# Optimization experiments

Measured on AMD Instinct MI355X. Metric: run time of the kernel, lower is better.

Reference implementation:

```python
import jax, jax.numpy as jnp
import numpy as np

B, N, D = 1, 10000, 256
NH, PT, PP, PS = 8, 4, 4, 4
DFF, NC, HF, WF = 1024, 6, 24, 60
BH, BW = 100, 100
T_RAD, S_RAD = 0.15, 0.12


def setup_inputs() -> dict:
    key = jax.random.key(0)
    ks = jax.random.split(key, 20)
    p = lambda i, shape: jax.random.normal(ks[i], shape, jnp.float32) * 0.02
    return {
        "query": jax.random.normal(ks[0], (B, N, D), jnp.float32),
        "prev_bev": jax.random.normal(ks[1], (B, N, D), jnp.float32),
        "image_feats": jax.random.normal(ks[2], (B, NC, D, HF, WF), jnp.float32),
        "reference_points_2d": jax.random.uniform(ks[3], (B, N, 2), jnp.float32),
        "reference_points_cam": jax.random.uniform(ks[4], (B, NC, N, PP, 2), jnp.float32),
        "ego_shift": jax.random.normal(ks[5], (B, 2), jnp.float32) * 0.02,
        "t_off_w": p(6, (2 * D, 2 * NH * PT * 2)), "t_off_b": jnp.zeros((2 * NH * PT * 2,)),
        "t_wt_w": p(7, (2 * D, 2 * NH * PT)), "t_wt_b": jnp.zeros((2 * NH * PT,)),
        "t_out_w": p(8, (D, D)), "t_out_b": jnp.zeros((D,)),
        "s_off_w": p(9, (D, NH * PP * PS * 2)), "s_off_b": jnp.zeros((NH * PP * PS * 2,)),
        "s_wt_w": p(10, (D, NH * PP * PS)), "s_wt_b": jnp.zeros((NH * PP * PS,)),
        "s_out_w": p(11, (D, D)), "s_out_b": jnp.zeros((D,)),
        "ffn_w1": p(12, (D, DFF)), "ffn_b1": jnp.zeros((DFF,)),
        "ffn_w2": p(13, (DFF, D)), "ffn_b2": jnp.zeros((D,)),
        "ln1_g": jnp.ones((D,)), "ln1_b": jnp.zeros((D,)),
        "ln2_g": jnp.ones((D,)), "ln2_b": jnp.zeros((D,)),
        "ln3_g": jnp.ones((D,)), "ln3_b": jnp.zeros((D,)),
        "bev_mask": jax.random.bernoulli(ks[14], 0.7, (B, NC, N, PP)),
        "bev_h": BH, "bev_w": BW,
    }


def _ln(x, g, b):
    mu = x.mean(-1, keepdims=True)
    var = ((x - mu) ** 2).mean(-1, keepdims=True)
    return (x - mu) / jnp.sqrt(var + 1e-5) * g + b


def _masked_softmax(logits, mask):
    m = mask.astype(logits.dtype)
    w = jax.nn.softmax(jnp.where(m == 0, -1e9, logits), axis=-1) * m
    return w / jnp.maximum(w.sum(-1, keepdims=True), 1e-6)


def _bilinear(feat, grid):
    # feat: [G, C, H, W]; grid: [G, Q, P, 2] in [-1, 1] (x, y); align_corners=False, zero pad
    G, C, H, W = feat.shape
    ix = ((grid[..., 0] + 1.0) * W - 1.0) * 0.5
    iy = ((grid[..., 1] + 1.0) * H - 1.0) * 0.5
    x0 = jnp.floor(ix); y0 = jnp.floor(iy)
    wx1 = ix - x0; wy1 = iy - y0
    feat_flat = feat.reshape(G, C, H * W)
    def corner(xc, yc, w):
        valid = (xc >= 0) & (xc < W) & (yc >= 0) & (yc < H)
        xi = jnp.clip(xc, 0, W - 1).astype(jnp.int32)
        yi = jnp.clip(yc, 0, H - 1).astype(jnp.int32)
        idx = (yi * W + xi).reshape(G, -1)
        vals = jax.vmap(lambda f, i: f[:, i])(feat_flat, idx)  # [G, C, Q*P]
        return vals * (w * valid.astype(feat.dtype)).reshape(G, 1, -1)
    out = (corner(x0, y0, (1 - wx1) * (1 - wy1)) + corner(x0 + 1, y0, wx1 * (1 - wy1))
           + corner(x0, y0 + 1, (1 - wx1) * wy1) + corner(x0 + 1, y0 + 1, wx1 * wy1))
    return out.reshape(G, C, grid.shape[1], grid.shape[2])


def _sample(fmap, pts, nh):
    # fmap: [B, C, H, W]; pts: [B, N, nh, P, 2] in [0, 1] -> [B, N, nh, P, hd]
    b, c, h, w = fmap.shape
    _, n, _, p, _ = pts.shape
    hd = c // nh
    feat = fmap.reshape(b * nh, hd, h, w)
    grid = jnp.transpose(pts, (0, 2, 1, 3, 4)).reshape(b * nh, n, p, 2) * 2.0 - 1.0
    s = _bilinear(feat, grid).reshape(b, nh, hd, n, p)
    return jnp.transpose(s, (0, 3, 1, 4, 2))


def _forward(query, prev_bev, image_feats, ref2d, refcam, ego_shift,
             t_off_w, t_off_b, t_wt_w, t_wt_b, t_out_w, t_out_b,
             s_off_w, s_off_b, s_wt_w, s_wt_b, s_out_w, s_out_b,
             ffn_w1, ffn_b1, ffn_w2, ffn_b2,
             ln1_g, ln1_b, ln2_g, ln2_b, ln3_g, ln3_b,
             bev_mask, bev_h, bev_w):
    b, n, d = query.shape
    nc = image_feats.shape[1]
    # ---- temporal self attention (pre-norm) ----
    q1 = _ln(query, ln1_g, ln1_b)
    pb = _ln(prev_bev, ln1_g, ln1_b)
    cur_map = jnp.transpose(q1, (0, 2, 1)).reshape(b, d, bev_h, bev_w)
    prev_map = jnp.transpose(pb, (0, 2, 1)).reshape(b, d, bev_h, bev_w)
    ai = jnp.concatenate([pb, q1], -1)
    toff = jnp.tanh(ai @ t_off_w + t_off_b).reshape(b, n, 2, NH, PT, 2) * T_RAD
    twl = (ai @ t_wt_w + t_wt_b).reshape(b, n, 2, NH, PT)
    base = jnp.stack([ref2d + ego_shift[:, None, :], ref2d], axis=2)
    t_outs = []
    for si, smap in enumerate((prev_map, cur_map)):
        loc = base[:, :, si, None, None, :] + toff[:, :, si]  # [b,n,NH,PT,2]
        w = jax.nn.softmax(twl[:, :, si], -1)
        s = _sample(smap, loc, NH)
        t_outs.append((s * w[..., None]).sum(3))  # [b,n,NH,hd]
    t_fused = ((t_outs[0] + t_outs[1]) * 0.5).reshape(b, n, d)
    x = query + (t_fused @ t_out_w + t_out_b)
    # ---- spatial cross attention (pre-norm) ----
    q2 = _ln(x, ln2_g, ln2_b)
    soff = jnp.tanh(q2 @ s_off_w + s_off_b).reshape(b, n, NH, PP, PS, 2) * S_RAD
    swl = (q2 @ s_wt_w + s_wt_b).reshape(b, n, NH, PP * PS)
    acc = jnp.zeros((b, n, d), query.dtype)
    cnt = jnp.zeros((b, n), query.dtype)
    for c in range(nc):
        ref = refcam[:, c]          # [b,n,PP,2]
        vis = bev_mask[:, c]        # [b,n,PP] bool
        loc = (ref[:, :, None, :, None, :] + soff).reshape(b, n, NH, PP * PS, 2)
        vm = jnp.broadcast_to(vis[:, :, None, :, None], (b, n, NH, PP, PS)).reshape(b, n, NH, PP * PS)
        w = _masked_softmax(swl, vm)
        s = _sample(image_feats[:, c], loc, NH)
        co = (s * w[..., None]).sum(3).reshape(b, n, d)
        hv = vis.any(-1)
        acc = acc + co * hv[..., None].astype(co.dtype)
        cnt = cnt + hv.astype(cnt.dtype)
    s_fused = acc / jnp.maximum(cnt, 1.0)[..., None]
    x = x + (s_fused @ s_out_w + s_out_b)
    # ---- FFN (pre-norm) ----
    h = jax.nn.relu(_ln(x, ln3_g, ln3_b) @ ffn_w1 + ffn_b1)
    return x + (h @ ffn_w2 + ffn_b2)


def reference(query, prev_bev, image_feats, reference_points_2d, reference_points_cam, ego_shift,
              t_off_w, t_off_b, t_wt_w, t_wt_b, t_out_w, t_out_b,
              s_off_w, s_off_b, s_wt_w, s_wt_b, s_out_w, s_out_b,
              ffn_w1, ffn_b1, ffn_w2, ffn_b2,
              ln1_g, ln1_b, ln2_g, ln2_b, ln3_g, ln3_b,
              bev_mask, bev_h, bev_w):
    return _forward(query, prev_bev, image_feats, reference_points_2d, reference_points_cam, ego_shift,
                    t_off_w, t_off_b, t_wt_w, t_wt_b, t_out_w, t_out_b,
                    s_off_w, s_off_b, s_wt_w, s_wt_b, s_out_w, s_out_b,
                    ffn_w1, ffn_b1, ffn_w2, ffn_b2,
                    ln1_g, ln1_b, ln2_g, ln2_b, ln3_g, ln3_b,
                    bev_mask, bev_h, bev_w)
```

## Files before the change

kernel.cpp:

```cpp
#include <hip/hip_runtime.h>
#include <hip/hip_bf16.h>
#include <hip/hip_fp16.h>

#define N_Q 10000
#define D_MODEL 256
#define NH 8
#define PT 4
#define PP 4
#define PS 4
#define DFF 1024
#define NC 6
#define HF 24
#define WF 60
#define BH 100
#define BW 100
#define T_RAD 0.15f
#define S_RAD 0.12f

typedef __hip_bfloat16 bf16;
typedef __attribute__((ext_vector_type(8))) short short8;
typedef __attribute__((ext_vector_type(4))) float f32x4;

__device__ __forceinline__ float b2f(bf16 v) { return __bfloat162float(v); }
__device__ __forceinline__ bf16 f2b(float v) { return __float2bfloat16(v); }

__device__ __forceinline__ f32x4 mfma16(short8 a, short8 b, f32x4 c) {
    return __builtin_amdgcn_mfma_f32_16x16x32_bf16(a, b, c, 0, 0, 0);
}

__device__ __forceinline__ float load_any(const void* p, long i, int f) {
    if (f == 0) return ((const float*)p)[i];
    if (f == 1) return b2f(((const bf16*)p)[i]);
    return __half2float(((const __half*)p)[i]);
}
__device__ __forceinline__ void store_any(void* p, long i, int f, float v) {
    if (f == 0)      ((float*)p)[i] = v;
    else if (f == 1) ((bf16*)p)[i] = f2b(v);
    else             ((__half*)p)[i] = __float2half(v);
}

__device__ __forceinline__ unsigned pack2(float a, float b) {
    bf16 x = f2b(a), y = f2b(b);
    unsigned short ux = *(unsigned short*)&x, uy = *(unsigned short*)&y;
    return (unsigned)ux | ((unsigned)uy << 16);
}

__global__ __launch_bounds__(256) void detect_kernel(const void* __restrict__ ln1g,
                                                     const void* __restrict__ mask,
                                                     int* __restrict__ flags) {
    __shared__ int sh[6];
    int tid = threadIdx.x;
    if (tid < 6) sh[tid] = (tid == 0 || tid == 2 || tid == 4) ? 1 : 0;
    __syncthreads();
    const unsigned long long* m64 = (const unsigned long long*)mask;
    const unsigned int*       m32 = (const unsigned int*)mask;
    const unsigned short*     m16 = (const unsigned short*)mask;
    int lok8 = 1, lones8 = 0, lok4 = 1, lones4 = 0, lok2 = 1, lones2 = 0;
    for (int i = tid; i < 480; i += 256) {
        if (i < 120) {
            unsigned long long v = m64[i];
            if (v == 1ULL) lones8++; else if (v != 0ULL) lok8 = 0;
        }
        if (i < 240) {
            unsigned int v = m32[i];
            if (v == 1u || v == 0x3F800000u) lones4++; else if (v != 0u) lok4 = 0;
        }
        unsigned short v = m16[i];
        if (v == 1 || v == 0x3F80) lones2++; else if (v != 0) lok2 = 0;
    }
    atomicAnd(&sh[0], lok8); atomicAdd(&sh[1], lones8);
    atomicAnd(&sh[2], lok4); atomicAdd(&sh[3], lones4);
    atomicAnd(&sh[4], lok2); atomicAdd(&sh[5], lones2);
    __syncthreads();
    if (tid == 0) {
        unsigned short u0 = ((const unsigned short*)ln1g)[0];
        flags[0] = (u0 == 0x3F80) ? 1 : (u0 == 0x3C00 ? 2 : 0);
        int ms;
        if (sh[0] && sh[1] > 30)       ms = 8;
        else if (sh[2] && sh[3] > 60)  ms = 4;
        else if (sh[4] && sh[5] > 120) ms = 2;
        else                           ms = 1;
        flags[1] = ms;
    }
}

#define NP 23
struct PrepDesc {
    const void* src[NP];
    int dst_off[NP];
    int count[NP];
    int R[NP];
    int C[NP];
    int type[NP];
    int blk_start[NP + 1];
};
__global__ __launch_bounds__(256) void prep_kernel(PrepDesc pd, bf16* __restrict__ wgt,
                                                   bf16* __restrict__ imgT,
                                                   const int* __restrict__ flags) {
    int blk = blockIdx.x;
    int a = 0;
    while (a < NP - 1 && blk >= pd.blk_start[a + 1]) a++;
    int i = (blk - pd.blk_start[a]) * 256 + threadIdx.x;
    if (i >= pd.count[a]) return;
    int f = flags[0];
    int ty = pd.type[a];
    if (ty == 0) {
        wgt[pd.dst_off[a] + i] = f2b(load_any(pd.src[a], i, f));
    } else if (ty == 1) {
        int R = pd.R[a], C = pd.C[a];
        int c = i / R, r = i % R;
        wgt[pd.dst_off[a] + i] = f2b(load_any(pd.src[a], (long)r * C + c, f));
    } else {
        int ch = i & 255;
        int t = i >> 8;
        int xx = t % WF; t /= WF;
        int yy = t % HF;
        int c  = t / HF;
        long src = (((long)(c * 256) + ch) * HF + yy) * WF + xx;
        imgT[i] = f2b(load_any(pd.src[a], src, f));
    }
}

__global__ __launch_bounds__(256) void ln12_kernel(const void* __restrict__ pb,
                                                   const void* __restrict__ q,
                                                   const int* __restrict__ flags,
                                                   const bf16* __restrict__ g,
                                                   const bf16* __restrict__ b,
                                                   bf16* __restrict__ out) {
    int wv = threadIdx.x >> 6, lane = threadIdx.x & 63;
    long row = (long)blockIdx.x * 4 + wv;
    const void* src; long r; int ooff;
    if (row < N_Q) { src = pb; r = row; ooff = 0; }
    else           { src = q;  r = row - N_Q; ooff = 256; }
    int f = flags[0];
    float v0, v1, v2, v3;
    if (f == 0) {
        float4 t = ((const float4*)src)[r * 64 + lane];
        v0 = t.x; v1 = t.y; v2 = t.z; v3 = t.w;
    } else {
        uint2 t = ((const uint2*)src)[r * 64 + lane];
        if (f == 1) {
            v0 = __uint_as_float(t.x << 16); v1 = __uint_as_float(t.x & 0xFFFF0000u);
            v2 = __uint_as_float(t.y << 16); v3 = __uint_as_float(t.y & 0xFFFF0000u);
        } else {
            __half2 h0 = *(__half2*)&t.x, h1 = *(__half2*)&t.y;
            v0 = __half2float(h0.x); v1 = __half2float(h0.y);
            v2 = __half2float(h1.x); v3 = __half2float(h1.y);
        }
    }
    float s1 = v0 + v1 + v2 + v3;
    float s2 = v0 * v0 + v1 * v1 + v2 * v2 + v3 * v3;
    #pragma unroll
    for (int m = 32; m > 0; m >>= 1) {
        s1 += __shfl_xor(s1, m);
        s2 += __shfl_xor(s2, m);
    }
    float mu = s1 * (1.f / 256.f);
    float var = s2 * (1.f / 256.f) - mu * mu;
    float inv = rsqrtf(var + 1e-5f);
    int k = lane * 4;
    float o0 = (v0 - mu) * inv * b2f(g[k+0]) + b2f(b[k+0]);
    float o1 = (v1 - mu) * inv * b2f(g[k+1]) + b2f(b[k+1]);
    float o2 = (v2 - mu) * inv * b2f(g[k+2]) + b2f(b[k+2]);
    float o3 = (v3 - mu) * inv * b2f(g[k+3]) + b2f(b[k+3]);
    uint2 st = {pack2(o0, o1), pack2(o2, o3)};
    *reinterpret_cast<uint2*>(out + r * 512 + ooff + k) = st;
}

__global__ __launch_bounds__(256) void ln_kernel(const float* __restrict__ in,
                                                 const bf16* __restrict__ g,
                                                 const bf16* __restrict__ b,
                                                 bf16* __restrict__ out) {
    int wv = threadIdx.x >> 6, lane = threadIdx.x & 63;
    long r = (long)blockIdx.x * 4 + wv;
    float4 t = ((const float4*)in)[r * 64 + lane];
    float s1 = t.x + t.y + t.z + t.w;
    float s2 = t.x * t.x + t.y * t.y + t.z * t.z + t.w * t.w;
    #pragma unroll
    for (int m = 32; m > 0; m >>= 1) {
        s1 += __shfl_xor(s1, m);
        s2 += __shfl_xor(s2, m);
    }
    float mu = s1 * (1.f / 256.f);
    float var = s2 * (1.f / 256.f) - mu * mu;
    float inv = rsqrtf(var + 1e-5f);
    int k = lane * 4;
    float o0 = (t.x - mu) * inv * b2f(g[k+0]) + b2f(b[k+0]);
    float o1 = (t.y - mu) * inv * b2f(g[k+1]) + b2f(b[k+1]);
    float o2 = (t.z - mu) * inv * b2f(g[k+2]) + b2f(b[k+2]);
    float o3 = (t.w - mu) * inv * b2f(g[k+3]) + b2f(b[k+3]);
    uint2 st = {pack2(o0, o1), pack2(o2, o3)};
    *reinterpret_cast<uint2*>(out + r * 256 + k) = st;
}

template <int K, int J, int MODE>
__global__ __launch_bounds__(256) void gemm_mfma(const bf16* __restrict__ A,
                                                 const bf16* __restrict__ WT,
                                                 const bf16* __restrict__ bias,
                                                 float* __restrict__ outf,
                                                 const void* __restrict__ resraw,
                                                 const float* __restrict__ resf,
                                                 const int* __restrict__ flags) {
    constexpr int LDK = K + 8;
    __shared__ bf16 As[32 * LDK];
    int tid = threadIdx.x;
    int row0 = blockIdx.x * 32;
    int col0 = blockIdx.y * 64;
    for (int t = tid; t < 32 * (K / 8); t += 256) {
        int r = t / (K / 8), kq = t % (K / 8);
        uint4 u = {0u, 0u, 0u, 0u};
        if (row0 + r < N_Q)
            u = *reinterpret_cast<const uint4*>(A + (size_t)(row0 + r) * K + kq * 8);
        *reinterpret_cast<uint4*>(&As[r * LDK + kq * 8]) = u;
    }
    __syncthreads();
    int wave = tid >> 6, lane = tid & 63;
    int l = lane & 15, quad = lane >> 4;
    int rh = wave >> 1, ch = wave & 1;
    constexpr int NK = K / 32;
    short8 afr[NK];
    const bf16* arow = &As[(rh * 16 + l) * LDK + quad * 8];
    #pragma unroll
    for (int ks = 0; ks < NK; ks++)
        afr[ks] = *reinterpret_cast<const short8*>(arow + ks * 32);
    int fdt = flags[0];
    #pragma unroll
    for (int ct = 0; ct < 2; ct++) {
        int col = col0 + ch * 32 + ct * 16 + l;
        const bf16* wrow = WT + (size_t)col * K + quad * 8;
        f32x4 acc = {0.f, 0.f, 0.f, 0.f};
        #pragma unroll
        for (int ks = 0; ks < NK; ks++) {
            short8 bfr = *reinterpret_cast<const short8*>(wrow + ks * 32);
            acc = mfma16(afr[ks], bfr, acc);
        }
        float bb = b2f(bias[col]);
        #pragma unroll
        for (int r = 0; r < 4; r++) {
            int row = row0 + rh * 16 + quad * 4 + r;
            if (row >= N_Q) continue;
            long o = (long)row * J + col;
            float v = acc[r] + bb;
            if (MODE == 2) outf[o] = v + load_any(resraw, o, fdt);
            else           outf[o] = v + resf[o];
        }
    }
}

template <int K, int J1, int J2>
__global__ __launch_bounds__(256) void gemm_dual(const bf16* __restrict__ A,
                                                 const bf16* __restrict__ WT1,
                                                 const bf16* __restrict__ b1, float scale,
                                                 bf16* __restrict__ out1,
                                                 const bf16* __restrict__ WT2,
                                                 const bf16* __restrict__ b2,
                                                 bf16* __restrict__ out2) {
    constexpr int LDK = K + 8;
    __shared__ bf16 As[32 * LDK];
    int tid = threadIdx.x;
    int row0 = blockIdx.x * 32;
    int col0 = blockIdx.y * 64;
    for (int t = tid; t < 32 * (K / 8); t += 256) {
        int r = t / (K / 8), kq = t % (K / 8);
        uint4 u = {0u, 0u, 0u, 0u};
        if (row0 + r < N_Q)
            u = *reinterpret_cast<const uint4*>(A + (size_t)(row0 + r) * K + kq * 8);
        *reinterpret_cast<uint4*>(&As[r * LDK + kq * 8]) = u;
    }
    __syncthreads();
    int wave = tid >> 6, lane = tid & 63;
    int l = lane & 15, quad = lane >> 4;
    int rh = wave >> 1, ch = wave & 1;
    constexpr int NK = K / 32;
    short8 afr[NK];
    const bf16* arow = &As[(rh * 16 + l) * LDK + quad * 8];
    #pragma unroll
    for (int ks = 0; ks < NK; ks++)
        afr[ks] = *reinterpret_cast<const short8*>(arow + ks * 32);
    #pragma unroll
    for (int ct = 0; ct < 2; ct++) {
        int jg = col0 + ch * 32 + ct * 16 + l;
        int in1 = jg < J1;
        int cl = in1 ? jg : jg - J1;
        const bf16* wrow = (in1 ? WT1 : WT2) + (size_t)cl * K + quad * 8;
        f32x4 acc = {0.f, 0.f, 0.f, 0.f};
        #pragma unroll
        for (int ks = 0; ks < NK; ks++) {
            short8 bfr = *reinterpret_cast<const short8*>(wrow + ks * 32);
            acc = mfma16(afr[ks], bfr, acc);
        }
        float bb = b2f(in1 ? b1[cl] : b2[cl]);
        #pragma unroll
        for (int r = 0; r < 4; r++) {
            int row = row0 + rh * 16 + quad * 4 + r;
            if (row >= N_Q) continue;
            float v = acc[r] + bb;
            if (in1) out1[(long)row * J1 + cl] = f2b(tanhf(v) * scale);
            else     out2[(long)row * J2 + cl] = f2b(v);
        }
    }
}

__global__ __launch_bounds__(256) void ffn_mfma(const float* __restrict__ x,
                                                const bf16* __restrict__ g3,
                                                const bf16* __restrict__ b3,
                                                const bf16* __restrict__ w1T,
                                                const bf16* __restrict__ b1,
                                                const bf16* __restrict__ w2T,
                                                const bf16* __restrict__ b2v,
                                                void* __restrict__ out,
                                                const int* __restrict__ flags) {
    constexpr int LDH = DFF + 8;
    constexpr int LDX = D_MODEL + 8;
    __shared__ bf16 hbuf[16 * LDH];
    bf16* xl = hbuf;
    int tid = threadIdx.x;
    int row0 = blockIdx.x * 16;
    {
        int r = tid >> 4, lr = tid & 15;
        const float* xr = x + (long)(row0 + r) * 256 + lr * 16;
        float vals[16];
        float s1 = 0.f, s2 = 0.f;
        #pragma unroll
        for (int i = 0; i < 16; i++) {
            float v = xr[i];
            vals[i] = v; s1 += v; s2 += v * v;
        }
        #pragma unroll
        for (int off = 8; off > 0; off >>= 1) {
            s1 += __shfl_down(s1, off, 16);
            s2 += __shfl_down(s2, off, 16);
        }
        s1 = __shfl(s1, 0, 16);
        s2 = __shfl(s2, 0, 16);
        float mu = s1 * (1.f / 256.f);
        float var = s2 * (1.f / 256.f) - mu * mu;
        float inv = rsqrtf(var + 1e-5f);
        #pragma unroll
        for (int i = 0; i < 16; i++) {
            int k = lr * 16 + i;
            xl[r * LDX + k] = f2b((vals[i] - mu) * inv * b2f(g3[k]) + b2f(b3[k]));
        }
    }
    __syncthreads();
    int wave = tid >> 6, lane = tid & 63;
    int l = lane & 15, quad = lane >> 4;
    short8 afr[8];
    {
        const bf16* arow = xl + l * LDX + quad * 8;
        #pragma unroll
        for (int ks = 0; ks < 8; ks++)
            afr[ks] = *reinterpret_cast<const short8*>(arow + ks * 32);
    }
    __syncthreads();
    for (int ct = 0; ct < 16; ct++) {
        int col = wave * 256 + ct * 16 + l;
        const bf16* wrow = w1T + (size_t)col * 256 + quad * 8;
        f32x4 acc = {0.f, 0.f, 0.f, 0.f};
        #pragma unroll
        for (int ks = 0; ks < 8; ks++) {
            short8 bfr = *reinterpret_cast<const short8*>(wrow + ks * 32);
            acc = mfma16(afr[ks], bfr, acc);
        }
        float bb = b2f(b1[col]);
        #pragma unroll
        for (int r = 0; r < 4; r++)
            hbuf[(quad * 4 + r) * LDH + col] = f2b(fmaxf(acc[r] + bb, 0.f));
    }
    __syncthreads();
    int fdt = flags[0];
    for (int ct = 0; ct < 4; ct++) {
        int col = wave * 64 + ct * 16 + l;
        const bf16* wrow = w2T + (size_t)col * 1024 + quad * 8;
        const bf16* hrow = hbuf + l * LDH + quad * 8;
        f32x4 acc = {0.f, 0.f, 0.f, 0.f};
        #pragma unroll 8
        for (int ks = 0; ks < 32; ks++) {
            short8 a2 = *reinterpret_cast<const short8*>(hrow + ks * 32);
            short8 bfr = *reinterpret_cast<const short8*>(wrow + ks * 32);
            acc = mfma16(a2, bfr, acc);
        }
        float bb = b2f(b2v[col]);
        #pragma unroll
        for (int r = 0; r < 4; r++) {
            long o = (long)(row0 + quad * 4 + r) * 256 + col;
            store_any(out, o, fdt, x[o] + acc[r] + bb);
        }
    }
}

__global__ __launch_bounds__(256) void temporal_kernel(const bf16* __restrict__ ai,
                                                       const bf16* __restrict__ toffB,
                                                       const bf16* __restrict__ twlB,
                                                       const void* __restrict__ ref2d,
                                                       const void* __restrict__ ego,
                                                       const int* __restrict__ flags,
                                                       bf16* __restrict__ tfB) {
    int tid = threadIdx.x;
    int ql = tid >> 5, t = tid & 31;
    int g = t >> 2, q4 = t & 3;
    long n0 = (long)blockIdx.x * 8;
    __shared__ float s_toff[8][8][17];
    __shared__ float s_twl[8][64];
    __shared__ float s_base[8][4];
    for (int i = tid; i < 8 * 128; i += 256) {
        int q = i >> 7, j = i & 127;
        int si = j >> 6, r = j & 63, gg = r >> 3, w = r & 7;
        s_toff[q][gg][si * 8 + w] = b2f(toffB[n0 * 128 + i]);
    }
    for (int i = tid; i < 8 * 64; i += 256) s_twl[i >> 6][i & 63] = b2f(twlB[n0 * 64 + i]);
    if (tid < 8) {
        int f = flags[0];
        float rx = load_any(ref2d, (n0 + tid) * 2, f), ry = load_any(ref2d, (n0 + tid) * 2 + 1, f);
        s_base[tid][0] = rx + load_any(ego, 0, f); s_base[tid][1] = ry + load_any(ego, 1, f);
        s_base[tid][2] = rx;                       s_base[tid][3] = ry;
    }
    __syncthreads();
    float acc[8];
    #pragma unroll
    for (int i = 0; i < 8; i++) acc[i] = 0.f;
    int choff = g * 32 + q4 * 8;
    #pragma unroll
    for (int si = 0; si < 2; si++) {
        float l0 = s_twl[ql][si * 32 + g * 4 + 0], l1 = s_twl[ql][si * 32 + g * 4 + 1];
        float l2 = s_twl[ql][si * 32 + g * 4 + 2], l3 = s_twl[ql][si * 32 + g * 4 + 3];
        float mx = fmaxf(fmaxf(l0, l1), fmaxf(l2, l3));
        float e0 = __expf(l0 - mx), e1 = __expf(l1 - mx);
        float e2 = __expf(l2 - mx), e3 = __expf(l3 - mx);
        float inv = 1.f / (e0 + e1 + e2 + e3);
        float wts[4] = {e0 * inv, e1 * inv, e2 * inv, e3 * inv};
        int aoff = si * 256;
        float bx = s_base[ql][si * 2], by = s_base[ql][si * 2 + 1];
        #pragma unroll
        for (int pt = 0; pt < 4; pt++) {
            float u = bx + s_toff[ql][g][si * 8 + pt * 2 + 0];
            float v = by + s_toff[ql][g][si * 8 + pt * 2 + 1];
            float ix = u * (float)BW - 0.5f;
            float iy = v * (float)BH - 0.5f;
            float x0f = floorf(ix), y0f = floorf(iy);
            int x0 = (int)x0f, y0 = (int)y0f;
            float wx1 = ix - x0f, wy1 = iy - y0f;
            float wx0 = 1.f - wx1, wy0 = 1.f - wy1;
            #pragma unroll
            for (int cy = 0; cy < 2; cy++) {
                int yy = y0 + cy;
                if ((unsigned)yy >= BH) continue;
                float wy = cy ? wy1 : wy0;
                #pragma unroll
                for (int cx = 0; cx < 2; cx++) {
                    int xx = x0 + cx;
                    if ((unsigned)xx >= BW) continue;
                    float wq = wts[pt] * wy * (cx ? wx1 : wx0);
                    uint4 uu = *reinterpret_cast<const uint4*>(
                        ai + (long)(yy * BW + xx) * 512 + aoff + choff);
                    acc[0] += wq * __uint_as_float(uu.x << 16);
                    acc[1] += wq * __uint_as_float(uu.x & 0xFFFF0000u);
                    acc[2] += wq * __uint_as_float(uu.y << 16);
                    acc[3] += wq * __uint_as_float(uu.y & 0xFFFF0000u);
                    acc[4] += wq * __uint_as_float(uu.z << 16);
                    acc[5] += wq * __uint_as_float(uu.z & 0xFFFF0000u);
                    acc[6] += wq * __uint_as_float(uu.w << 16);
                    acc[7] += wq * __uint_as_float(uu.w & 0xFFFF0000u);
                }
            }
        }
    }
    uint4 o;
    o.x = pack2(acc[0] * 0.5f, acc[1] * 0.5f);
    o.y = pack2(acc[2] * 0.5f, acc[3] * 0.5f);
    o.z = pack2(acc[4] * 0.5f, acc[5] * 0.5f);
    o.w = pack2(acc[6] * 0.5f, acc[7] * 0.5f);
    *reinterpret_cast<uint4*>(tfB + (n0 + ql) * 256 + choff) = o;
}

__global__ __launch_bounds__(256) void spatial_kernel(const bf16* __restrict__ soffB,
                                                      const bf16* __restrict__ swlB,
                                                      const void* __restrict__ refcam,
                                                      const void* __restrict__ bmask,
                                                      const bf16* __restrict__ imgT,
                                                      const void* __restrict__ img_raw,
                                                      int use_imgT,
                                                      const int* __restrict__ flags,
                                                      bf16* __restrict__ sfB) {
    int tid = threadIdx.x;
    int ql = tid >> 6, lane = tid & 63;
    int cxh = lane >> 5;
    int h5 = lane & 31;
    int g = h5 >> 2, c8 = h5 & 3;
    long n0 = (long)blockIdx.x * 4;
    __shared__ float s_soff[4][8][33];
    __shared__ float s_swl[4][144];
    __shared__ float s_ref[4][NC][PP][2];
    __shared__ int   s_vis[4][NC][PP];
    for (int i = tid; i < 4 * 256; i += 256) {
        int q = i >> 8, j = i & 255;
        s_soff[q][j >> 5][j & 31] = b2f(soffB[n0 * 256 + i]);
    }
    for (int i = tid; i < 4 * 128; i += 256) {
        int q = i >> 7, jr = i & 127;
        int gg = jr >> 4, j = jr & 15;
        s_swl[q][j * 9 + gg] = b2f(swlB[n0 * 128 + i]);
    }
    int fdt = flags[0], msz = flags[1];
    if (tid < 4 * 48) {
        int q = tid / 48, r = tid % 48;
        s_ref[q][r >> 3][(r & 7) >> 1][r & 1] =
            load_any(refcam, ((long)(r >> 3) * N_Q + n0 + q) * 8 + (r & 7), fdt);
    }
    if (tid >= 160 && tid < 160 + 4 * 24) {
        int tt = tid - 160;
        int q = tt / 24, r = tt % 24; int c = r >> 2, p = r & 3;
        long idx = ((long)c * N_Q + n0 + q) * 4 + p;
        int v;
        if (msz == 1)      v = ((const unsigned char*)bmask)[idx] != 0;
        else if (msz == 2) v = ((const unsigned short*)bmask)[idx] != 0;
        else if (msz == 4) v = ((const unsigned int*)bmask)[idx] != 0u;
        else               v = ((const unsigned long long*)bmask)[idx] != 0ULL;
        s_vis[q][c][p] = v;
    }
    __syncthreads();
    float ew[16];
    {
        float lw[16], mx = -3e38f;
        #pragma unroll
        for (int j = 0; j < 16; j++) { lw[j] = s_swl[ql][j * 9 + g]; mx = fmaxf(mx, lw[j]); }
        #pragma unroll
        for (int j = 0; j < 16; j++) ew[j] = __expf(lw[j] - mx);
    }
    float acc[8];
    #pragma unroll
    for (int i = 0; i < 8; i++) acc[i] = 0.f;
    float cnt = 0.f;
    int choff = g * 32 + c8 * 8;
    for (int c = 0; c < NC; c++) {
        int m0 = s_vis[ql][c][0], m1 = s_vis[ql][c][1];
        int m2 = s_vis[ql][c][2], m3 = s_vis[ql][c][3];
        if (!(m0 | m1 | m2 | m3)) continue;
        cnt += 1.f;
        float sum = 0.f;
        #pragma unroll
        for (int j = 0; j < 16; j++)
            sum += s_vis[ql][c][j >> 2] ? ew[j] : 0.f;
        float inv = 1.f / fmaxf(sum, 1e-20f);
        const bf16* img = imgT + (long)c * HF * WF * 256 + choff;
        #pragma unroll
        for (int p = 0; p < PP; p++) {
            if (!s_vis[ql][c][p]) continue;
            float rx = s_ref[ql][c][p][0], ry = s_ref[ql][c][p][1];
            #pragma unroll
            for (int s = 0; s < PS; s++) {
                float wi = ew[p * 4 + s] * inv;
                float u = rx + s_soff[ql][g][p * 8 + s * 2 + 0];
                float v = ry + s_soff[ql][g][p * 8 + s * 2 + 1];
                float ix = u * (float)WF - 0.5f, iy = v * (float)HF - 0.5f;
                float x0f = floorf(ix), y0f = floorf(iy);
                int x0 = (int)x0f, y0 = (int)y0f;
                float wx1 = ix - x0f, wy1 = iy - y0f;
                int xi = x0 + cxh;
                float wx = cxh ? wx1 : (1.f - wx1);
                wx *= ((unsigned)xi < WF) ? 1.f : 0.f;
                int xcl = min(max(xi, 0), WF - 1);
                float wiwx = wi * wx;
                #pragma unroll
                for (int cy = 0; cy < 2; cy++) {
                    int yy = y0 + cy;
                    if ((unsigned)yy >= HF) continue;
                    float wq = wiwx * (cy ? wy1 : (1.f - wy1));
                    if (use_imgT) {
                        uint4 uu = *reinterpret_cast<const uint4*>(
                            img + (long)(yy * WF + xcl) * 256);
                        acc[0] += wq * __uint_as_float(uu.x << 16);
                        acc[1] += wq * __uint_as_float(uu.x & 0xFFFF0000u);
                        acc[2] += wq * __uint_as_float(uu.y << 16);
                        acc[3] += wq * __uint_as_float(uu.y & 0xFFFF0000u);
                        acc[4] += wq * __uint_as_float(uu.z << 16);
                        acc[5] += wq * __uint_as_float(uu.z & 0xFFFF0000u);
                        acc[6] += wq * __uint_as_float(uu.w << 16);
                        acc[7] += wq * __uint_as_float(uu.w & 0xFFFF0000u);
                    } else {
                        #pragma unroll
                        for (int e = 0; e < 8; e++)
                            acc[e] += wq * load_any(img_raw,
                                (((long)c * 256 + choff + e) * HF + yy) * WF + xcl, fdt);
                    }
                }
            }
        }
    }
    #pragma unroll
    for (int e = 0; e < 8; e++) acc[e] += __shfl_xor(acc[e], 32);
    float invc = 1.f / fmaxf(cnt, 1.f);
    if (cxh == 0) {
        uint4 o;
        o.x = pack2(acc[0] * invc, acc[1] * invc);
        o.y = pack2(acc[2] * invc, acc[3] * invc);
        o.z = pack2(acc[4] * invc, acc[5] * invc);
        o.w = pack2(acc[6] * invc, acc[7] * invc);
        *reinterpret_cast<uint4*>(sfB + (n0 + ql) * 256 + choff) = o;
    }
}

#define W_TOFF_W 0
#define W_TOFF_B 65536
#define W_TWT_W  65664
#define W_TWT_B  98432
#define W_TOUT_W 98496
#define W_TOUT_B 164032
#define W_SOFF_W 164288
#define W_SOFF_B 229824
#define W_SWT_W  230080
#define W_SWT_B  262848
#define W_SOUT_W 262976
#define W_SOUT_B 328512
#define W_FFN_W1 328768
#define W_FFN_B1 590912
#define W_FFN_W2 591936
#define W_FFN_B2 854080
#define W_LN1_G  854336
#define W_LN1_B  854592
#define W_LN2_G  854848
#define W_LN2_B  855104
#define W_LN3_G  855360
#define W_LN3_B  855616

#define OB_WGT   0
#define OB_FLAGS 1711744
#define OB_AI    1712640
#define OB_TF    11952640
#define OB_X     17072640
#define OB_T4    27312640
#define OB_IMG   31152640
#define WS_NEED_IMG 35576320ULL

extern "C" void kernel_launch(void* const* d_in, const int* in_sizes, int n_in,
                              void* d_out, int out_size, void* d_ws, size_t ws_size,
                              hipStream_t stream) {
    char* W8 = (char*)d_ws;
    bf16*  wgt   = (bf16*)(W8 + OB_WGT);
    int*   flags = (int*)(W8 + OB_FLAGS);
    bf16*  ai    = (bf16*)(W8 + OB_AI);
    bf16*  q2B   = ai;
    bf16*  sfB   = (bf16*)(W8 + OB_AI + 5120000);
    bf16*  tfB   = (bf16*)(W8 + OB_TF);
    bf16*  soffB = tfB;
    float* x     = (float*)(W8 + OB_X);
    bf16*  toffB = (bf16*)(W8 + OB_T4);
    bf16*  twlB  = (bf16*)(W8 + OB_T4 + 2560000);
    bf16*  swlB  = toffB;
    bf16*  imgT  = (bf16*)(W8 + OB_IMG);
    int use_imgT = (ws_size >= WS_NEED_IMG) ? 1 : 0;

    detect_kernel<<<1, 256, 0, stream>>>(d_in[22], d_in[28], flags);

    {
        PrepDesc pd;
        const int tsrc[8] = {6, 8, 10, 12, 14, 16, 18, 20};
        const int toff[8] = {W_TOFF_W, W_TWT_W, W_TOUT_W, W_SOFF_W, W_SWT_W, W_SOUT_W,
                             W_FFN_W1, W_FFN_W2};
        const int tR[8] = {512, 512, 256, 256, 256, 256, 256, 1024};
        const int tC[8] = {128, 64, 256, 256, 128, 256, 1024, 256};
        const int fsrc[14] = {7, 9, 11, 13, 15, 17, 19, 21, 22, 23, 24, 25, 26, 27};
        const int foff[14] = {W_TOFF_B, W_TWT_B, W_TOUT_B, W_SOFF_B, W_SWT_B, W_SOUT_B,
                              W_FFN_B1, W_FFN_B2, W_LN1_G, W_LN1_B, W_LN2_G, W_LN2_B,
                              W_LN3_G, W_LN3_B};
        const int fcnt[14] = {128, 64, 256, 256, 128, 256, 1024, 256, 256, 256, 256, 256, 256, 256};
        int a = 0, blk = 0;
        for (int i = 0; i < 8; i++, a++) {
            pd.src[a] = d_in[tsrc[i]]; pd.dst_off[a] = toff[i];
            pd.count[a] = tR[i] * tC[i]; pd.R[a] = tR[i]; pd.C[a] = tC[i];
            pd.type[a] = 1; pd.blk_start[a] = blk; blk += (pd.count[a] + 255) / 256;
        }
        for (int i = 0; i < 14; i++, a++) {
            pd.src[a] = d_in[fsrc[i]]; pd.dst_off[a] = foff[i];
            pd.count[a] = fcnt[i]; pd.R[a] = 0; pd.C[a] = 0;
            pd.type[a] = 0; pd.blk_start[a] = blk; blk += (pd.count[a] + 255) / 256;
        }
        pd.src[a] = d_in[2]; pd.dst_off[a] = 0;
        pd.count[a] = use_imgT ? NC * HF * WF * 256 : 0;
        pd.R[a] = 0; pd.C[a] = 0; pd.type[a] = 2; pd.blk_start[a] = blk;
        blk += (pd.count[a] + 255) / 256;
        pd.blk_start[NP] = blk;
        prep_kernel<<<blk, 256, 0, stream>>>(pd, wgt, imgT, flags);
    }

    ln12_kernel<<<5000, 256, 0, stream>>>(d_in[1], d_in[0], flags,
                                          wgt + W_LN1_G, wgt + W_LN1_B, ai);
    gemm_dual<512, 128, 64><<<dim3(313, 3), 256, 0, stream>>>(ai,
        wgt + W_TOFF_W, wgt + W_TOFF_B, T_RAD, toffB,
        wgt + W_TWT_W, wgt + W_TWT_B, twlB);
    temporal_kernel<<<1250, 256, 0, stream>>>(ai, toffB, twlB, d_in[3], d_in[5], flags, tfB);
    gemm_mfma<256, 256, 2><<<dim3(313, 4), 256, 0, stream>>>(tfB, wgt + W_TOUT_W, wgt + W_TOUT_B,
        x, d_in[0], nullptr, flags);
    ln_kernel<<<2500, 256, 0, stream>>>(x, wgt + W_LN2_G, wgt + W_LN2_B, q2B);
    gemm_dual<256, 256, 128><<<dim3(313, 6), 256, 0, stream>>>(q2B,
        wgt + W_SOFF_W, wgt + W_SOFF_B, S_RAD, soffB,
        wgt + W_SWT_W, wgt + W_SWT_B, swlB);
    spatial_kernel<<<2500, 256, 0, stream>>>(soffB, swlB, d_in[4], d_in[28], imgT, d_in[2],
                                             use_imgT, flags, sfB);
    gemm_mfma<256, 256, 3><<<dim3(313, 4), 256, 0, stream>>>(sfB, wgt + W_SOUT_W, wgt + W_SOUT_B,
        x, nullptr, x, flags);
    ffn_mfma<<<625, 256, 0, stream>>>(x, wgt + W_LN3_G, wgt + W_LN3_B,
                                      wgt + W_FFN_W1, wgt + W_FFN_B1,
                                      wgt + W_FFN_W2, wgt + W_FFN_B2, d_out, flags);
}
```

Before: 473.2 us.

## Precompute spatial sampling records cooperatively in shared memory to cut redundant address math

The spatial cross-attention gather kernel used to have every lane recompute the softmax weights, per-camera normalisation and bilinear coordinates for all 16 samples, although 8 lanes per head share them. Now the softmax exponentials and per-camera inverse sums are computed once into shared memory. For each camera, each thread builds two packed sample records (corner coordinates, x fraction, y-weighted attention weights), which the gather loop then reads. The WF/HF scale and the -0.5 shift are also folded into the staged offsets and reference points. This cuts ALU work per lane but adds two block barriers per camera iteration and extra shared-memory traffic.

```diff
diff --git a/kernel.cpp b/kernel.cpp
--- a/kernel.cpp
+++ b/kernel.cpp
@@ -492,9 +492,12 @@
     __shared__ float s_swl[4][144];
     __shared__ float s_ref[4][NC][PP][2];
     __shared__ int   s_vis[4][NC][PP];
+    __shared__ float s_ew[4][8][16];
+    __shared__ float s_inv[4][8][NC];
+    __shared__ float4 s_rec[4][16][8];
     for (int i = tid; i < 4 * 256; i += 256) {
         int q = i >> 8, j = i & 255;
-        s_soff[q][j >> 5][j & 31] = b2f(soffB[n0 * 256 + i]);
+        s_soff[q][j >> 5][j & 31] = b2f(soffB[n0 * 256 + i]) * ((j & 1) ? (float)HF : (float)WF);
     }
     for (int i = tid; i < 4 * 128; i += 256) {
         int q = i >> 7, jr = i & 127;
@@ -504,8 +507,9 @@
     int fdt = flags[0], msz = flags[1];
     if (tid < 4 * 48) {
         int q = tid / 48, r = tid % 48;
+        float sc = (r & 1) ? (float)HF : (float)WF;
         s_ref[q][r >> 3][(r & 7) >> 1][r & 1] =
-            load_any(refcam, ((long)(r >> 3) * N_Q + n0 + q) * 8 + (r & 7), fdt);
+            load_any(refcam, ((long)(r >> 3) * N_Q + n0 + q) * 8 + (r & 7), fdt) * sc - 0.5f;
     }
     if (tid >= 160 && tid < 160 + 4 * 24) {
         int tt = tid - 160;
@@ -519,73 +523,101 @@
         s_vis[q][c][p] = v;
     }
     __syncthreads();
-    float ew[16];
-    {
+    if (tid < 32) {
+        int q = tid >> 3, gg = tid & 7;
         float lw[16], mx = -3e38f;
         #pragma unroll
-        for (int j = 0; j < 16; j++) { lw[j] = s_swl[ql][j * 9 + g]; mx = fmaxf(mx, lw[j]); }
-        #pragma unroll
-        for (int j = 0; j < 16; j++) ew[j] = __expf(lw[j] - mx);
-    }
+        for (int j = 0; j < 16; j++) { lw[j] = s_swl[q][j * 9 + gg]; mx = fmaxf(mx, lw[j]); }
+        #pragma unroll
+        for (int j = 0; j < 16; j++) s_ew[q][gg][j] = __expf(lw[j] - mx);
+    }
+    __syncthreads();
+    if (tid < 192) {
+        int c = tid % NC, gq = tid / NC;
+        int q = gq >> 3, gg = gq & 7;
+        float sum = 0.f;
+        #pragma unroll
+        for (int j = 0; j < 16; j++)
+            sum += s_vis[q][c][j >> 2] ? s_ew[q][gg][j] : 0.f;
+        s_inv[q][gg][c] = 1.f / fmaxf(sum, 1e-20f);
+    }
+    __syncthreads();
+
     float acc[8];
     #pragma unroll
     for (int i = 0; i < 8; i++) acc[i] = 0.f;
     float cnt = 0.f;
     int choff = g * 32 + c8 * 8;
+    int choffB = choff * 2;
+    int rec = tid * 2;
+    int rq = rec >> 7, rg = (rec >> 4) & 7, rp = (rec >> 2) & 3, rs0 = rec & 3;
     for (int c = 0; c < NC; c++) {
+        if (s_vis[rq][c][rp]) {
+            float invv = s_inv[rq][rg][c];
+            float rx = s_ref[rq][c][rp][0], ry = s_ref[rq][c][rp][1];
+            #pragma unroll
+            for (int ds = 0; ds < 2; ds++) {
+                int s = rs0 + ds;
+                float wi = s_ew[rq][rg][rp * 4 + s] * invv;
+                float ix = rx + s_soff[rq][rg][rp * 8 + s * 2 + 0];
+                float iy = ry + s_soff[rq][rg][rp * 8 + s * 2 + 1];
+                float x0f = floorf(ix), y0f = floorf(iy);
+                float wx1 = ix - x0f, wy1 = iy - y0f;
+                int x0 = (int)x0f, y0 = (int)y0f;
+                float4 rr;
+                rr.x = __int_as_float((x0 + 8) | ((y0 + 8) << 16));
+                rr.y = wx1;
+                rr.z = wi * (1.f - wy1);
+                rr.w = wi * wy1;
+                s_rec[rq][rp * 4 + s][rg] = rr;
+            }
+        }
+        __syncthreads();
         int m0 = s_vis[ql][c][0], m1 = s_vis[ql][c][1];
         int m2 = s_vis[ql][c][2], m3 = s_vis[ql][c][3];
-        if (!(m0 | m1 | m2 | m3)) continue;
-        cnt += 1.f;
-        float sum = 0.f;
-        #pragma unroll
-        for (int j = 0; j < 16; j++)
-            sum += s_vis[ql][c][j >> 2] ? ew[j] : 0.f;
-        float inv = 1.f / fmaxf(sum, 1e-20f);
-        const bf16* img = imgT + (long)c * HF * WF * 256 + choff;
-        #pragma unroll
-        for (int p = 0; p < PP; p++) {
-            if (!s_vis[ql][c][p]) continue;
-            float rx = s_ref[ql][c][p][0], ry = s_ref[ql][c][p][1];
+        if (m0 | m1 | m2 | m3) {
+            cnt += 1.f;
+            const char* imgc = (const char*)imgT + (size_t)c * (HF * WF * 512) + choffB;
             #pragma unroll
-            for (int s = 0; s < PS; s++) {
-                float wi = ew[p * 4 + s] * inv;
-                float u = rx + s_soff[ql][g][p * 8 + s * 2 + 0];
-                float v = ry + s_soff[ql][g][p * 8 + s * 2 + 1];
-                float ix = u * (float)WF - 0.5f, iy = v * (float)HF - 0.5f;
-                float x0f = floorf(ix), y0f = floorf(iy);
-                int x0 = (int)x0f, y0 = (int)y0f;
-                float wx1 = ix - x0f, wy1 = iy - y0f;
-                int xi = x0 + cxh;
-                float wx = cxh ? wx1 : (1.f - wx1);
-                wx *= ((unsigned)xi < WF) ? 1.f : 0.f;
-                int xcl = min(max(xi, 0), WF - 1);
-                float wiwx = wi * wx;
+            for (int p = 0; p < PP; p++) {
+                if (!s_vis[ql][c][p]) continue;
                 #pragma unroll
-                for (int cy = 0; cy < 2; cy++) {
-                    int yy = y0 + cy;
-                    if ((unsigned)yy >= HF) continue;
-                    float wq = wiwx * (cy ? wy1 : (1.f - wy1));
-                    if (use_imgT) {
-                        uint4 uu = *reinterpret_cast<const uint4*>(
-                            img + (long)(yy * WF + xcl) * 256);
-                        acc[0] += wq * __uint_as_float(uu.x << 16);
-                        acc[1] += wq * __uint_as_float(uu.x & 0xFFFF0000u);
-                        acc[2] += wq * __uint_as_float(uu.y << 16);
-                        acc[3] += wq * __uint_as_float(uu.y & 0xFFFF0000u);
-                        acc[4] += wq * __uint_as_float(uu.z << 16);
-                        acc[5] += wq * __uint_as_float(uu.z & 0xFFFF0000u);
-                        acc[6] += wq * __uint_as_float(uu.w << 16);
-                        acc[7] += wq * __uint_as_float(uu.w & 0xFFFF0000u);
-                    } else {
-                        #pragma unroll
-                        for (int e = 0; e < 8; e++)
-                            acc[e] += wq * load_any(img_raw,
-                                (((long)c * 256 + choff + e) * HF + yy) * WF + xcl, fdt);
+                for (int s = 0; s < PS; s++) {
+                    float4 rc = s_rec[ql][p * 4 + s][g];
+                    int xy = __float_as_int(rc.x);
+                    int x0 = (xy & 0xFFFF) - 8;
+                    int y0 = (xy >> 16) - 8;
+                    int xi = x0 + cxh;
+                    float wx = cxh ? rc.y : 1.f - rc.y;
+                    wx = ((unsigned)xi < WF) ? wx : 0.f;
+                    int xcl = min(max(xi, 0), WF - 1);
+                    const char* colp = imgc + xcl * 512;
+                    #pragma unroll
+                    for (int cy = 0; cy < 2; cy++) {
+                        int yy = y0 + cy;
+                        if ((unsigned)yy >= HF) continue;
+                        float wq = wx * (cy ? rc.w : rc.z);
+                        if (use_imgT) {
+                            uint4 uu = *reinterpret_cast<const uint4*>(colp + yy * (WF * 512));
+                            acc[0] += wq * __uint_as_float(uu.x << 16);
+                            acc[1] += wq * __uint_as_float(uu.x & 0xFFFF0000u);
+                            acc[2] += wq * __uint_as_float(uu.y << 16);
+                            acc[3] += wq * __uint_as_float(uu.y & 0xFFFF0000u);
+                            acc[4] += wq * __uint_as_float(uu.z << 16);
+                            acc[5] += wq * __uint_as_float(uu.z & 0xFFFF0000u);
+                            acc[6] += wq * __uint_as_float(uu.w << 16);
+                            acc[7] += wq * __uint_as_float(uu.w & 0xFFFF0000u);
+                        } else {
+                            #pragma unroll
+                            for (int e = 0; e < 8; e++)
+                                acc[e] += wq * load_any(img_raw,
+                                    (((long)c * 256 + choff + e) * HF + yy) * WF + xcl, fdt);
+                        }
                     }
                 }
             }
         }
+        __syncthreads();
     }
     #pragma unroll
     for (int e = 0; e < 8; e++) acc[e] += __shfl_xor(acc[e], 32);
```

After: 487.6 us. 1.03x slower.
